# Performance work log

Measured on AMD Instinct MI355X. Metric: run time of the kernel, lower is better.

## Reference

```python
import jax, jax.numpy as jnp
import numpy as np

D_MODEL = 1024
NUM_HEADS = 16
D_HEAD = D_MODEL // NUM_HEADS


def _rope(x):
    """Rotary embedding, lucidrains interleaved convention, applied along axis -2.

    x: (..., n, d). Positions are arange(n); freq_i = 10000**(-2i/d), each freq
    repeated twice (interleaved); rotate_half swaps adjacent pairs (-x2, x1).
    """
    n, d = x.shape[-2], x.shape[-1]
    inv_freq = 1.0 / (10000.0 ** (jnp.arange(0, d, 2, dtype=jnp.float32) / d))  # (d/2,)
    freqs = jnp.arange(n, dtype=jnp.float32)[:, None] * inv_freq[None, :]       # (n, d/2)
    emb = jnp.repeat(freqs, 2, axis=-1)                                         # (n, d)
    cos, sin = jnp.cos(emb).astype(x.dtype), jnp.sin(emb).astype(x.dtype)
    xp = x.reshape(x.shape[:-1] + (d // 2, 2))
    rot = jnp.stack([-xp[..., 1], xp[..., 0]], axis=-1).reshape(x.shape)
    return x * cos + rot * sin


def setup_inputs() -> dict:
    key = jax.random.key(0)
    ks = jax.random.split(key, 11)
    B, S = 4, 2048
    mk = lambda k, shape: (jax.random.normal(k, shape, dtype=jnp.float32) * 0.02)
    return {
        "query": jax.random.normal(ks[0], (B, S, D_MODEL), dtype=jnp.float32),
        "key": jax.random.normal(ks[1], (B, S, D_MODEL), dtype=jnp.float32),
        "value": jax.random.normal(ks[2], (B, S, D_MODEL), dtype=jnp.float32),
        "Wq": mk(ks[3], (D_MODEL, D_MODEL)), "bq": jnp.zeros((D_MODEL,), jnp.float32),
        "Wk": mk(ks[4], (D_MODEL, D_MODEL)), "bk": jnp.zeros((D_MODEL,), jnp.float32),
        "Wv": mk(ks[5], (D_MODEL, D_MODEL)), "bv": jnp.zeros((D_MODEL,), jnp.float32),
        "Wo": mk(ks[6], (D_MODEL, D_MODEL)), "bo": jnp.zeros((D_MODEL,), jnp.float32),
    }


def reference(query, key, value, Wq, bq, Wk, bk, Wv, bv, Wo, bo):
    B, S, _ = query.shape
    H, dh = NUM_HEADS, D_HEAD
    # projections (torch Linear: x @ W.T + b)
    q = (query @ Wq.T + bq).reshape(B, S, H, dh)           # (b, t, h, d)
    k = (key @ Wk.T + bk).reshape(B, S, H, dh).transpose(0, 2, 1, 3)   # (b, h, t, d)
    v = (value @ Wv.T + bv).reshape(B, S, H, dh).transpose(0, 2, 1, 3)  # (b, h, t, d)
    # Faithful to source: query rotated along axis -2 = HEADS axis (pre-permute),
    # key rotated along axis -2 = time axis.
    q = _rope(q)                                            # positions over heads (source quirk)
    k = _rope(k)                                            # positions over time
    q = q.transpose(0, 2, 1, 3)                             # (b, h, t, d)
    scores = jnp.einsum("bhqd,bhkd->bhqk", q, k) / jnp.sqrt(jnp.float32(D_MODEL))
    attn = jax.nn.softmax(scores, axis=-1)
    ctx = jnp.einsum("bhqk,bhkd->bhqd", attn, v)            # (b, h, t, d)
    ctx = ctx.transpose(0, 2, 1, 3).reshape(B, S, H * dh)   # (b, t, d_model)
    return ctx @ Wo.T + bo
```

## Files before the change

### kernel.cpp

```cpp
#include <hip/hip_runtime.h>

using u16 = unsigned short;
typedef __bf16 bf16x8 __attribute__((ext_vector_type(8)));
typedef __bf16 bf16x2 __attribute__((ext_vector_type(2)));
typedef float f32x4 __attribute__((ext_vector_type(4)));

#if __has_builtin(__builtin_amdgcn_exp2f)
#define QSCALE 0.04508422468443852f
#define FEXP(x) __builtin_amdgcn_exp2f(x)
#else
#define QSCALE 0.03125f
#define FEXP(x) __expf(x)
#endif

__device__ __forceinline__ u16 f2bf(float f) {
  unsigned u = __builtin_bit_cast(unsigned, f);
  u += 0x7FFFu + ((u >> 16) & 1u);
  return (u16)(u >> 16);
}

#define GLD_LDS16(g, l)                                                                   \
  __builtin_amdgcn_global_load_lds((const __attribute__((address_space(1))) void*)(g),    \
                                   (__attribute__((address_space(3))) void*)(l), 16, 0, 0)

template <int LOG2NB>
__global__ void cvt_multi(const float* __restrict__ i0, const float* __restrict__ i1,
                          const float* __restrict__ i2, const float* __restrict__ i3,
                          u16* __restrict__ o0, u16* __restrict__ o1, u16* __restrict__ o2,
                          u16* __restrict__ o3, int n4) {
  const int which = blockIdx.x >> LOG2NB;
  const float* in = which == 0 ? i0 : which == 1 ? i1 : which == 2 ? i2 : i3;
  u16* out = which == 0 ? o0 : which == 1 ? o1 : which == 2 ? o2 : o3;
  int i = (blockIdx.x & ((1 << LOG2NB) - 1)) * blockDim.x + threadIdx.x;
  const int st = (1 << LOG2NB) * blockDim.x;
  for (; i < n4; i += st) {
    float4 v = reinterpret_cast<const float4*>(in)[i];
    ushort4 o = make_ushort4(f2bf(v.x), f2bf(v.y), f2bf(v.z), f2bf(v.w));
    reinterpret_cast<ushort4*>(out)[i] = o;
  }
}

template <int EPI>
__global__ __launch_bounds__(512, 4) void gemm_bt(const u16* __restrict__ A,
                                                  const u16* __restrict__ Bt,
                                                  const float* __restrict__ bias,
                                                  void* __restrict__ outp) {
  __shared__ u16 lA[3][128 * 32];
  __shared__ u16 lB[3][128 * 32];
  const int tid = threadIdx.x;
  const int l = tid & 63, w = tid >> 6;
  const int wr = w >> 2, wc = w & 3;
  const int l15 = l & 15, lg = l >> 4;
  const int rsw = (l15 >> 1) & 3;
  const int bid = ((blockIdx.x & 7) << 6) | (blockIdx.x >> 3);
  const int br = bid >> 3, bc = bid & 7;

  f32x4 acc[4][2];
#pragma unroll
  for (int m = 0; m < 4; ++m)
#pragma unroll
    for (int n = 0; n < 2; ++n) acc[m][n] = f32x4{0.f, 0.f, 0.f, 0.f};

  const int srow = tid >> 2;
  const int gch = (tid & 3) ^ ((tid >> 3) & 3);
  const u16* Abase = A + (size_t)(br * 128 + srow) * 1024 + gch * 8;
  const u16* Bbase = Bt + (size_t)(bc * 128 + srow) * 1024 + gch * 8;

  auto stage = [&](int buf, int kk) {
    GLD_LDS16(Abase + kk, &lA[buf][tid * 8]);
    GLD_LDS16(Bbase + kk, &lB[buf][tid * 8]);
  };

  auto compute = [&](int cur) {
    const int c = ((lg ^ rsw) << 3);
    bf16x8 af[4], bfr[2];
#pragma unroll
    for (int m = 0; m < 4; ++m)
      af[m] = *reinterpret_cast<const bf16x8*>(&lA[cur][(wr * 64 + m * 16 + l15) * 32 + c]);
#pragma unroll
    for (int n = 0; n < 2; ++n)
      bfr[n] = *reinterpret_cast<const bf16x8*>(&lB[cur][(wc * 32 + n * 16 + l15) * 32 + c]);
#pragma unroll
    for (int m = 0; m < 4; ++m)
#pragma unroll
      for (int n = 0; n < 2; ++n)
        acc[m][n] = __builtin_amdgcn_mfma_f32_16x16x32_bf16(af[m], bfr[n], acc[m][n], 0, 0, 0);
  };

  stage(0, 0);
  stage(1, 32);
  asm volatile("s_waitcnt vmcnt(2)" ::: "memory");
  __builtin_amdgcn_s_barrier();
  __builtin_amdgcn_sched_barrier(0);

  int cur = 0, nx2 = 2;
  for (int it = 0; it < 31; ++it) {
    if (it < 30) stage(nx2, (it + 2) * 32);
    compute(cur);
    if (it < 30)
      asm volatile("s_waitcnt vmcnt(2)" ::: "memory");
    else
      asm volatile("s_waitcnt vmcnt(0)" ::: "memory");
    __builtin_amdgcn_s_barrier();
    __builtin_amdgcn_sched_barrier(0);
    cur = cur == 2 ? 0 : cur + 1;
    nx2 = nx2 == 2 ? 0 : nx2 + 1;
  }
  compute(cur);

  const int row0 = br * 128 + wr * 64;
  const int col0 = bc * 128 + wc * 32;

  if constexpr (EPI == 0 || EPI == 1) {
    u16* out = reinterpret_cast<u16*>(outp);
#pragma unroll
    for (int n = 0; n < 2; ++n) {
      const int gn = col0 + n * 16 + l15;
      const float bv2 = bias[gn];
      const int p = (gn & 63) >> 1;
      const float invf = __expf((float)p * -0.28782313663f);
      float ss = 0.f, cc = 0.f;
      if constexpr (EPI == 0) {
        const float th = (float)(gn >> 6) * invf;
        sincosf(th, &ss, &cc);
      }
#pragma unroll
      for (int m = 0; m < 4; ++m) {
        const int gm0 = row0 + m * 16 + lg * 4;
#pragma unroll
        for (int r = 0; r < 4; ++r) {
          float x = acc[m][n][r] + bv2;
          if constexpr (EPI == 1) {
            const float th = (float)((gm0 + r) & 2047) * invf;
            sincosf(th, &ss, &cc);
          }
          const float xp = __shfl_xor(x, 1);
          float o = (gn & 1) ? fmaf(xp, ss, x * cc) : fmaf(-xp, ss, x * cc);
          if constexpr (EPI == 0) o *= QSCALE;
          out[(size_t)(gm0 + r) * 1024 + gn] = f2bf(o);
        }
      }
    }
  } else if constexpr (EPI == 2) {
    u16* vT = reinterpret_cast<u16*>(outp);
#pragma unroll
    for (int n = 0; n < 2; ++n) {
      const int gn = col0 + n * 16 + l15;
      const float bv2 = bias[gn];
      const int hh = gn >> 6, dd = gn & 63;
#pragma unroll
      for (int m = 0; m < 4; ++m) {
        const int gm0 = row0 + m * 16 + lg * 4;
        const int bb = gm0 >> 11, s0 = gm0 & 2047;
        ushort4 pk = make_ushort4(f2bf(acc[m][n][0] + bv2), f2bf(acc[m][n][1] + bv2),
                                  f2bf(acc[m][n][2] + bv2), f2bf(acc[m][n][3] + bv2));
        *reinterpret_cast<ushort4*>(vT + ((size_t)((bb * 16 + hh) * 64 + dd) * 2048 + s0)) = pk;
      }
    }
  } else {
    float* out = reinterpret_cast<float*>(outp);
#pragma unroll
    for (int n = 0; n < 2; ++n) {
      const int gn = col0 + n * 16 + l15;
      const float bv2 = bias[gn];
#pragma unroll
      for (int m = 0; m < 4; ++m) {
        const int gm0 = row0 + m * 16 + lg * 4;
#pragma unroll
        for (int r = 0; r < 4; ++r) out[(size_t)(gm0 + r) * 1024 + gn] = acc[m][n][r] + bv2;
      }
    }
  }
}

__global__ __launch_bounds__(512, 8) void attn_fwd(const u16* __restrict__ Q,
                                                   const u16* __restrict__ K,
                                                   const u16* __restrict__ Vt,
                                                   u16* __restrict__ ctx) {
  __shared__ u16 sK[2][64 * 64];
  __shared__ u16 sV[2][64 * 64];
  const int tid = threadIdx.x;
  const int l = tid & 63, w = tid >> 6;
  const int l15 = l & 15, lg = l >> 4;
  const int swz = (l15 & 7) << 3;
  const int wgid = ((blockIdx.x & 7) << 7) | (blockIdx.x >> 3);
  const int qt = wgid & 15, bh = wgid >> 4;
  const int b = bh >> 4, h = bh & 15;

  bf16x8 qf0, qf1;
  {
    const u16* qp = Q + (size_t)(b * 2048 + qt * 128 + w * 16 + l15) * 1024 + h * 64 + lg * 8;
    qf0 = *reinterpret_cast<const bf16x8*>(qp);
    qf1 = *reinterpret_cast<const bf16x8*>(qp + 32);
  }

  float l_i = 0.f;
  f32x4 acc_o[4];
#pragma unroll
  for (int n = 0; n < 4; ++n) acc_o[n] = f32x4{0.f, 0.f, 0.f, 0.f};

  const int srow = tid >> 3;
  const int scol = ((tid & 7) ^ (srow & 7)) * 8;
  const int krow = (srow & 0x23) | ((srow & 0x0C) << 1) | ((srow & 0x10) >> 2);
  const u16* Kbase = K + (size_t)(b * 2048 + krow) * 1024 + h * 64 + scol;
  const u16* Vbase = Vt + (size_t)(bh * 64 + srow) * 2048 + scol;

  auto stage = [&](int buf, int j) {
    GLD_LDS16(Kbase + (size_t)(j * 64) * 1024, &sK[buf][tid * 8]);
    GLD_LDS16(Vbase + j * 64, &sV[buf][tid * 8]);
  };

  stage(0, 0);
  __syncthreads();

  for (int j = 0; j < 32; ++j) {
    const int cur = j & 1;
    if (j < 31) stage(cur ^ 1, j + 1);

    f32x4 accs[4];
#pragma unroll
    for (int nk = 0; nk < 4; ++nk) accs[nk] = f32x4{0.f, 0.f, 0.f, 0.f};
    const int c0 = (lg * 8) ^ swz;
    __builtin_amdgcn_s_setprio(1);
#pragma unroll
    for (int nk = 0; nk < 4; ++nk) {
      bf16x8 kf0 = *reinterpret_cast<const bf16x8*>(&sK[cur][(nk * 16 + l15) * 64 + c0]);
      bf16x8 kf1 = *reinterpret_cast<const bf16x8*>(&sK[cur][(nk * 16 + l15) * 64 + (c0 ^ 32)]);
      accs[nk] = __builtin_amdgcn_mfma_f32_16x16x32_bf16(kf0, qf0, accs[nk], 0, 0, 0);
      accs[nk] = __builtin_amdgcn_mfma_f32_16x16x32_bf16(kf1, qf1, accs[nk], 0, 0, 0);
    }
    __builtin_amdgcn_s_setprio(0);

    float rs = 0.f;
    unsigned wpk[4][2];
#pragma unroll
    for (int nk = 0; nk < 4; ++nk) {
      const float p0 = FEXP(accs[nk][0]), p1 = FEXP(accs[nk][1]);
      const float p2 = FEXP(accs[nk][2]), p3 = FEXP(accs[nk][3]);
      rs += (p0 + p1) + (p2 + p3);
      bf16x2 t0, t1;
      t0.x = (__bf16)p0; t0.y = (__bf16)p1;
      t1.x = (__bf16)p2; t1.y = (__bf16)p3;
      wpk[nk][0] = __builtin_bit_cast(unsigned, t0);
      wpk[nk][1] = __builtin_bit_cast(unsigned, t1);
    }
    rs += __shfl_xor(rs, 16);
    rs += __shfl_xor(rs, 32);
    l_i += rs;

    __builtin_amdgcn_s_setprio(1);
#pragma unroll
    for (int ks = 0; ks < 2; ++ks) {
      const uint4 paw = make_uint4(wpk[2 * ks][0], wpk[2 * ks][1],
                                   wpk[2 * ks + 1][0], wpk[2 * ks + 1][1]);
      const bf16x8 pa = __builtin_bit_cast(bf16x8, paw);
#pragma unroll
      for (int n = 0; n < 4; ++n) {
        bf16x8 vf = *reinterpret_cast<const bf16x8*>(
            &sV[cur][(n * 16 + l15) * 64 + ((ks * 32 + lg * 8) ^ swz)]);
        acc_o[n] = __builtin_amdgcn_mfma_f32_16x16x32_bf16(vf, pa, acc_o[n], 0, 0, 0);
      }
    }
    __builtin_amdgcn_s_setprio(0);
    __syncthreads();
  }

  const float inv = 1.f / l_i;
  u16* obase = ctx + (size_t)(b * 2048 + qt * 128 + w * 16 + l15) * 1024 + h * 64;
#pragma unroll
  for (int n = 0; n < 4; ++n) {
    ushort4 pk = make_ushort4(f2bf(acc_o[n][0] * inv), f2bf(acc_o[n][1] * inv),
                              f2bf(acc_o[n][2] * inv), f2bf(acc_o[n][3] * inv));
    *reinterpret_cast<ushort4*>(obase + n * 16 + lg * 4) = pk;
  }
}

extern "C" void kernel_launch(void* const* d_in, const int* in_sizes, int n_in, void* d_out,
                              int out_size, void* d_ws, size_t ws_size, hipStream_t stream) {
  (void)in_sizes; (void)n_in; (void)out_size; (void)ws_size;
  const float* query = (const float*)d_in[0];
  const float* key = (const float*)d_in[1];
  const float* value = (const float*)d_in[2];
  const float* Wq = (const float*)d_in[3];
  const float* bq = (const float*)d_in[4];
  const float* Wk = (const float*)d_in[5];
  const float* bk = (const float*)d_in[6];
  const float* Wv = (const float*)d_in[7];
  const float* bv = (const float*)d_in[8];
  const float* Wo = (const float*)d_in[9];
  const float* bo = (const float*)d_in[10];

  char* ws = (char*)d_ws;
  const size_t MB = (size_t)1 << 20;
  u16* xq = (u16*)(ws + 0 * MB);
  u16* xk = (u16*)(ws + 16 * MB);
  u16* xv = (u16*)(ws + 32 * MB);
  u16* wqb = (u16*)(ws + 48 * MB);
  u16* wkb = (u16*)(ws + 50 * MB);
  u16* wvb = (u16*)(ws + 52 * MB);
  u16* wob = (u16*)(ws + 54 * MB);
  u16* qb = (u16*)(ws + 56 * MB);
  u16* kb = (u16*)(ws + 72 * MB);
  u16* vT = (u16*)(ws + 88 * MB);
  u16* cx = (u16*)(ws + 104 * MB);

  cvt_multi<9><<<1536, 256, 0, stream>>>(query, key, value, query, xq, xk, xv, xq, 2097152);
  cvt_multi<6><<<256, 256, 0, stream>>>(Wq, Wk, Wv, Wo, wqb, wkb, wvb, wob, 262144);

  gemm_bt<0><<<512, 512, 0, stream>>>(xq, wqb, bq, qb);
  gemm_bt<1><<<512, 512, 0, stream>>>(xk, wkb, bk, kb);
  gemm_bt<2><<<512, 512, 0, stream>>>(xv, wvb, bv, vT);
  attn_fwd<<<1024, 512, 0, stream>>>(qb, kb, vT, cx);
  gemm_bt<3><<<512, 512, 0, stream>>>(cx, wob, bo, (float*)d_out);
}
```

Measured before the change: 229.5 us.

## Triple-buffer K/V staging with vmcnt waits and compute row sums via MFMA

Moves attention K/V staging from double to triple buffering, prefetching two tiles ahead. The full __syncthreads is replaced by explicit s_waitcnt vmcnt plus s_barrier, so loads can overlap across more iterations. The per-row softmax denominator now comes from an extra MFMA against a ones vector, dropping the scalar adds and cross-lane shuffles. In exchange the kernel uses 1.5x the LDS and lowers the launch-bounds occupancy hint from 8 to 6, and the row sum is taken from the bf16-rounded probabilities.

```diff
diff --git a/kernel.cpp b/kernel.cpp
--- a/kernel.cpp
+++ b/kernel.cpp
@@ -173,12 +173,12 @@
   }
 }
 
-__global__ __launch_bounds__(512, 8) void attn_fwd(const u16* __restrict__ Q,
+__global__ __launch_bounds__(512, 6) void attn_fwd(const u16* __restrict__ Q,
                                                    const u16* __restrict__ K,
                                                    const u16* __restrict__ Vt,
                                                    u16* __restrict__ ctx) {
-  __shared__ u16 sK[2][64 * 64];
-  __shared__ u16 sV[2][64 * 64];
+  __shared__ u16 sK[3][64 * 64];
+  __shared__ u16 sV[3][64 * 64];
   const int tid = threadIdx.x;
   const int l = tid & 63, w = tid >> 6;
   const int l15 = l & 15, lg = l >> 4;
@@ -194,7 +194,11 @@
     qf1 = *reinterpret_cast<const bf16x8*>(qp + 32);
   }
 
-  float l_i = 0.f;
+  bf16x8 ones;
+#pragma unroll
+  for (int i = 0; i < 8; ++i) ones[i] = (__bf16)1.0f;
+
+  f32x4 acc_l = f32x4{0.f, 0.f, 0.f, 0.f};
   f32x4 acc_o[4];
 #pragma unroll
   for (int n = 0; n < 4; ++n) acc_o[n] = f32x4{0.f, 0.f, 0.f, 0.f};
@@ -211,11 +215,14 @@
   };
 
   stage(0, 0);
-  __syncthreads();
-
+  stage(1, 1);
+  asm volatile("s_waitcnt vmcnt(2)" ::: "memory");
+  __builtin_amdgcn_s_barrier();
+  __builtin_amdgcn_sched_barrier(0);
+
+  int cur = 0, nx2 = 2;
   for (int j = 0; j < 32; ++j) {
-    const int cur = j & 1;
-    if (j < 31) stage(cur ^ 1, j + 1);
+    if (j < 30) stage(nx2, j + 2);
 
     f32x4 accs[4];
 #pragma unroll
@@ -231,22 +238,17 @@
     }
     __builtin_amdgcn_s_setprio(0);
 
-    float rs = 0.f;
     unsigned wpk[4][2];
 #pragma unroll
     for (int nk = 0; nk < 4; ++nk) {
       const float p0 = FEXP(accs[nk][0]), p1 = FEXP(accs[nk][1]);
       const float p2 = FEXP(accs[nk][2]), p3 = FEXP(accs[nk][3]);
-      rs += (p0 + p1) + (p2 + p3);
       bf16x2 t0, t1;
       t0.x = (__bf16)p0; t0.y = (__bf16)p1;
       t1.x = (__bf16)p2; t1.y = (__bf16)p3;
       wpk[nk][0] = __builtin_bit_cast(unsigned, t0);
       wpk[nk][1] = __builtin_bit_cast(unsigned, t1);
     }
-    rs += __shfl_xor(rs, 16);
-    rs += __shfl_xor(rs, 32);
-    l_i += rs;
 
     __builtin_amdgcn_s_setprio(1);
 #pragma unroll
@@ -254,6 +256,7 @@
       const uint4 paw = make_uint4(wpk[2 * ks][0], wpk[2 * ks][1],
                                    wpk[2 * ks + 1][0], wpk[2 * ks + 1][1]);
       const bf16x8 pa = __builtin_bit_cast(bf16x8, paw);
+      acc_l = __builtin_amdgcn_mfma_f32_16x16x32_bf16(ones, pa, acc_l, 0, 0, 0);
 #pragma unroll
       for (int n = 0; n < 4; ++n) {
         bf16x8 vf = *reinterpret_cast<const bf16x8*>(
@@ -262,10 +265,20 @@
       }
     }
     __builtin_amdgcn_s_setprio(0);
-    __syncthreads();
-  }
-
-  const float inv = 1.f / l_i;
+
+    if (j < 31) {
+      if (j < 30)
+        asm volatile("s_waitcnt vmcnt(2)" ::: "memory");
+      else
+        asm volatile("s_waitcnt vmcnt(0)" ::: "memory");
+      __builtin_amdgcn_s_barrier();
+      __builtin_amdgcn_sched_barrier(0);
+    }
+    cur = cur == 2 ? 0 : cur + 1;
+    nx2 = nx2 == 2 ? 0 : nx2 + 1;
+  }
+
+  const float inv = 1.f / acc_l[0];
   u16* obase = ctx + (size_t)(b * 2048 + qt * 128 + w * 16 + l15) * 1024 + h * 64;
 #pragma unroll
   for (int n = 0; n < 4; ++n) {
```

New measurement: 218.3 us. 1.05x faster.
